# Kernel tuning notes

Measured on AMD Instinct MI355X. Metric: run time of the kernel, lower is better.

The kernel has to match this reference:

```python
import jax, jax.numpy as jnp
import numpy as np

E = 512      # embed_dim
H = 256      # hidden_dim
NH = 4       # num_heads
NC = 5       # num_classes
DH = H // NH # head_dim


def layer_norm(x, g, b, eps=1e-5):
    mu = jnp.mean(x, axis=-1, keepdims=True)
    var = jnp.mean((x - mu) ** 2, axis=-1, keepdims=True)
    return (x - mu) * jax.lax.rsqrt(var + eps) * g + b


def mha_seq1(q_in, kv_in, in_w, in_b, out_w, out_b):
    # q_in, kv_in: [B, H]; in_w: [3H, H]; seq_len == 1 for both query and key/value.
    wq, wk, wv = jnp.split(in_w, 3, axis=0)
    bq, bk, bv = jnp.split(in_b, 3, axis=0)
    B = q_in.shape[0]
    q = (q_in @ wq.T + bq).reshape(B, NH, DH)
    k = (kv_in @ wk.T + bk).reshape(B, NH, DH)
    v = (kv_in @ wv.T + bv).reshape(B, NH, DH)
    scores = jnp.sum(q * k, axis=-1) / jnp.sqrt(jnp.asarray(DH, q.dtype))  # [B, NH]
    w = jax.nn.softmax(scores[..., None], axis=-1)  # [B, NH, 1] (softmax over 1 key == 1)
    attn = (w * v).reshape(B, H)                    # [B, H]
    out = attn @ out_w.T + out_b
    weights = jnp.mean(w, axis=1)[:, None, :]       # [B, 1, 1], averaged over heads
    return out, weights


def setup_inputs() -> dict:
    key = jax.random.key(0)
    ks = jax.random.split(key, 16)
    s = lambda n: 1.0 / np.sqrt(n)
    d = {
        "image_feat": jax.random.normal(ks[0], (65536, E), jnp.float32),
        "text_feat": jax.random.normal(ks[1], (65536, E), jnp.float32),
        "img_proj_w": jax.random.normal(ks[2], (H, E), jnp.float32) * s(E),
        "img_proj_b": jnp.zeros((H,), jnp.float32),
        "txt_proj_w": jax.random.normal(ks[3], (H, E), jnp.float32) * s(E),
        "txt_proj_b": jnp.zeros((H,), jnp.float32),
        "t2i_in_w": jax.random.normal(ks[4], (3 * H, H), jnp.float32) * s(H),
        "t2i_in_b": jnp.zeros((3 * H,), jnp.float32),
        "t2i_out_w": jax.random.normal(ks[5], (H, H), jnp.float32) * s(H),
        "t2i_out_b": jnp.zeros((H,), jnp.float32),
        "i2t_in_w": jax.random.normal(ks[6], (3 * H, H), jnp.float32) * s(H),
        "i2t_in_b": jnp.zeros((3 * H,), jnp.float32),
        "i2t_out_w": jax.random.normal(ks[7], (H, H), jnp.float32) * s(H),
        "i2t_out_b": jnp.zeros((H,), jnp.float32),
        "norm1_g": jnp.ones((H,), jnp.float32),
        "norm1_b": jnp.zeros((H,), jnp.float32),
        "norm2_g": jnp.ones((H,), jnp.float32),
        "norm2_b": jnp.zeros((H,), jnp.float32),
        "cls_ln_g": jnp.ones((2 * H,), jnp.float32),
        "cls_ln_b": jnp.zeros((2 * H,), jnp.float32),
        "cls_w1": jax.random.normal(ks[8], (H, 2 * H), jnp.float32) * s(2 * H),
        "cls_b1": jnp.zeros((H,), jnp.float32),
        "cls_w2": jax.random.normal(ks[9], (NC, H), jnp.float32) * s(H),
        "cls_b2": jnp.zeros((NC,), jnp.float32),
    }
    return d


def reference(image_feat, text_feat, img_proj_w, img_proj_b, txt_proj_w, txt_proj_b,
              t2i_in_w, t2i_in_b, t2i_out_w, t2i_out_b,
              i2t_in_w, i2t_in_b, i2t_out_w, i2t_out_b,
              norm1_g, norm1_b, norm2_g, norm2_b,
              cls_ln_g, cls_ln_b, cls_w1, cls_b1, cls_w2, cls_b2):
    img = image_feat @ img_proj_w.T + img_proj_b   # [B, H]
    txt = text_feat @ txt_proj_w.T + txt_proj_b    # [B, H]
    txt_attn, txt_weights = mha_seq1(txt, img, t2i_in_w, t2i_in_b, t2i_out_w, t2i_out_b)
    txt_attn = layer_norm(txt + txt_attn, norm1_g, norm1_b)
    img_attn, img_weights = mha_seq1(img, txt, i2t_in_w, i2t_in_b, i2t_out_w, i2t_out_b)
    img_attn = layer_norm(img + img_attn, norm2_g, norm2_b)
    fused = jnp.concatenate([txt_attn, img_attn], axis=-1)  # [B, 2H]
    h = layer_norm(fused, cls_ln_g, cls_ln_b)
    h = jax.nn.gelu(h @ cls_w1.T + cls_b1, approximate=False)  # dropout is identity in eval
    out = h @ cls_w2.T + cls_b2                                 # [B, NC]
    return (out, txt_weights, img_weights)
```

## Files before the change

### kernel.cpp

```cpp
#include <hip/hip_runtime.h>
#include <cstdint>
#include <cstddef>


typedef unsigned short u16;
typedef __attribute__((ext_vector_type(8))) short bf16x8;
typedef __attribute__((ext_vector_type(4))) float f32x4;

__device__ __forceinline__ float bf2f(u16 u) {
  union { unsigned int i; float f; } v; v.i = ((unsigned int)u) << 16; return v.f;
}
__device__ __forceinline__ u16 f2bf(float f) {
  union { float f; unsigned int i; } v; v.f = f;
  unsigned int r = v.i + 0x7FFFu + ((v.i >> 16) & 1u);
  return (u16)(r >> 16);
}
__device__ __forceinline__ float ldf(const void* b, long long i, int bf) {
  if (bf) return bf2f(((const u16*)b)[i]);
  return ((const float*)b)[i];
}
__device__ __forceinline__ uint4 load8(const void* base, long long eoff, int bf) {
  if (bf) return *(const uint4*)((const u16*)base + eoff);
  const float* p = (const float*)base + eoff;
  float4 a = *(const float4*)p;
  float4 b = *(const float4*)(p + 4);
  union { u16 h[8]; uint4 u; } t;
  t.h[0] = f2bf(a.x); t.h[1] = f2bf(a.y); t.h[2] = f2bf(a.z); t.h[3] = f2bf(a.w);
  t.h[4] = f2bf(b.x); t.h[5] = f2bf(b.y); t.h[6] = f2bf(b.z); t.h[7] = f2bf(b.w);
  return t.u;
}

__global__ void kd_detect(const void* probe, int* flag) {
  if (threadIdx.x == 0 && blockIdx.x == 0) {
    unsigned int w = *(const unsigned int*)probe;
    *flag = (w == 0x3F803F80u) ? 1 : 0;
  }
}

__global__ void k0_T(const void* t2i_w, const void* i2t_w,
                     const void* img_w, const void* txt_w,
                     const void* img_b, const void* txt_b,
                     const void* t2i_b, const void* i2t_b,
                     float* __restrict__ T, float* __restrict__ cv, const int* dflag)
{
  const int bf = *dflag;
  int t = blockIdx.x * 256 + threadIdx.x;
  int mat = t >> 17;
  int j = (t >> 9) & 255;
  int k = t & 511;
  const void* wv = mat ? i2t_w : t2i_w;
  const void* wp = mat ? txt_w : img_w;
  float s = 0.f;
  #pragma unroll 8
  for (int i = 0; i < 256; ++i)
    s += ldf(wv, 512 * 256 + j * 256 + i, bf) * ldf(wp, i * 512 + k, bf);
  T[(size_t)t] = s;
  if (t < 512) {
    int m2 = t >> 8, j2 = t & 255;
    const void* wv2 = m2 ? i2t_w : t2i_w;
    const void* pb  = m2 ? txt_b : img_b;
    const void* ib  = m2 ? i2t_b : t2i_b;
    float s2 = 0.f;
    for (int i = 0; i < 256; ++i)
      s2 += ldf(wv2, 512 * 256 + j2 * 256 + i, bf) * ldf(pb, i, bf);
    cv[t] = s2 + ldf(ib, 512 + j2, bf);
  }
}

__global__ void k1_P(const void* txt_w, const void* img_w,
                     const void* t2i_ow, const void* i2t_ow,
                     const void* txt_b, const void* img_b,
                     const void* t2i_ob, const void* i2t_ob,
                     const float* __restrict__ T, const float* __restrict__ cv,
                     u16* __restrict__ P, float* __restrict__ c, const int* dflag)
{
  const int bf = *dflag;
  int t = blockIdx.x * 256 + threadIdx.x;
  int n = t >> 10;
  int k = t & 1023;
  u16 val;
  if (n < 256) {
    if (k < 512) {
      val = f2bf(ldf(txt_w, n * 512 + k, bf));
    } else {
      int kk = k - 512;
      float s = 0.f;
      #pragma unroll 8
      for (int j = 0; j < 256; ++j) s += ldf(t2i_ow, n * 256 + j, bf) * T[j * 512 + kk];
      val = f2bf(s);
    }
  } else {
    int n2 = n - 256;
    if (k < 512) {
      float s = 0.f;
      #pragma unroll 8
      for (int j = 0; j < 256; ++j) s += ldf(i2t_ow, n2 * 256 + j, bf) * T[256 * 512 + j * 512 + k];
      val = f2bf(s);
    } else {
      val = f2bf(ldf(img_w, n2 * 512 + (k - 512), bf));
    }
  }
  P[(size_t)n * 1024 + k] = val;
  if (k == 0) {
    float s;
    if (n < 256) {
      s = ldf(txt_b, n, bf) + ldf(t2i_ob, n, bf);
      for (int j = 0; j < 256; ++j) s += ldf(t2i_ow, n * 256 + j, bf) * cv[j];
    } else {
      int n2 = n - 256;
      s = ldf(img_b, n2, bf) + ldf(i2t_ob, n2, bf);
      for (int j = 0; j < 256; ++j) s += ldf(i2t_ow, n2 * 256 + j, bf) * cv[256 + j];
    }
    c[n] = s;
  }
}

__global__ __launch_bounds__(512, 4) void k2f(
    const void* txt, const void* img,
    const u16* __restrict__ P, const float* __restrict__ c,
    const void* g1, const void* b1, const void* g2, const void* b2,
    const void* gc, const void* bc,
    const void* W1, const void* b1c, const void* W2, const void* b2c,
    void* out, const int* dflag)
{
  const int bf = *dflag;
  __shared__ __align__(16) union {
    u16 As[64 * 64];
    u16 F[64 * 512];
  } sm;
  __shared__ float cb[512];
  __shared__ float part[8][64][5];

  const int tid = threadIdx.x;
  const int lane = tid & 63, wid = tid >> 6;
  const int fr = lane & 15, fq = lane >> 4;
  const int bm = blockIdx.x;
  const int wn = wid * 64;

  cb[tid] = c[tid];

  f32x4 acc[4][4];
  const f32x4 zero = {0.f, 0.f, 0.f, 0.f};
  #pragma unroll
  for (int i = 0; i < 4; ++i)
    #pragma unroll
    for (int j = 0; j < 4; ++j) acc[i][j] = zero;

  const int arow = tid >> 3, ac16 = tid & 7;
  for (int k0 = 0; k0 < 1024; k0 += 64) {
    const void* src = (k0 < 512) ? txt : img;
    const int kk = k0 & 511;
    {
      uint4 v = load8(src, (long long)(bm * 64 + arow) * 512 + kk + ac16 * 8, bf);
      ((uint4*)sm.As)[arow * 8 + (ac16 ^ (arow & 7))] = v;
    }
    __syncthreads();
    #pragma unroll
    for (int ks = 0; ks < 64; ks += 32) {
      bf16x8 af[4], bfr[4];
      #pragma unroll
      for (int i = 0; i < 4; ++i) {
        int row = i * 16 + fr;
        af[i] = *(const bf16x8*)((const char*)sm.As + row * 128 +
                                 ((ks * 2 + fq * 16) ^ ((row & 7) << 4)));
      }
      #pragma unroll
      for (int j = 0; j < 4; ++j)
        bfr[j] = *(const bf16x8*)&P[(size_t)(wn + j * 16 + fr) * 1024 + k0 + ks + fq * 8];
      #pragma unroll
      for (int i = 0; i < 4; ++i)
        #pragma unroll
        for (int j = 0; j < 4; ++j)
          acc[i][j] = __builtin_amdgcn_mfma_f32_16x16x32_bf16(af[i], bfr[j], acc[i][j], 0, 0, 0);
    }
    __syncthreads();
  }

  float bj[4];
  #pragma unroll
  for (int j = 0; j < 4; ++j) bj[j] = cb[wn + j * 16 + fr];
  #pragma unroll
  for (int i = 0; i < 4; ++i)
    #pragma unroll
    for (int j = 0; j < 4; ++j)
      #pragma unroll
      for (int r = 0; r < 4; ++r)
        sm.F[(size_t)(i * 16 + fq * 4 + r) * 512 + wn + j * 16 + fr] =
            f2bf(acc[i][j][r] + bj[j]);
  __syncthreads();

  const int c0 = lane * 8;
  const void* gh = (lane >= 32) ? g2 : g1;
  const void* bh = (lane >= 32) ? b2 : b1;
  const int hofs = (lane & 31) * 8;
  float ga8[8], ba8[8], gc8[8], bc8[8];
  #pragma unroll
  for (int i = 0; i < 8; ++i) {
    ga8[i] = ldf(gh, hofs + i, bf);
    ba8[i] = ldf(bh, hofs + i, bf);
    gc8[i] = ldf(gc, c0 + i, bf);
    bc8[i] = ldf(bc, c0 + i, bf);
  }
  for (int rr = 0; rr < 8; ++rr) {
    const int row = wid * 8 + rr;
    uint4 raw = *(const uint4*)&sm.F[(size_t)row * 512 + c0];
    const u16* rp = (const u16*)&raw;
    float x[8];
    #pragma unroll
    for (int i = 0; i < 8; ++i) x[i] = bf2f(rp[i]);
    float s = 0.f, ss = 0.f;
    #pragma unroll
    for (int i = 0; i < 8; ++i) { s += x[i]; ss += x[i] * x[i]; }
    #pragma unroll
    for (int m = 1; m <= 16; m <<= 1) { s += __shfl_xor(s, m, 64); ss += __shfl_xor(ss, m, 64); }
    float mu = s * (1.f / 256.f);
    float var = ss * (1.f / 256.f) - mu * mu;
    float rstd = rsqrtf(var + 1e-5f);
    float y[8]; float s2 = 0.f, ss2 = 0.f;
    #pragma unroll
    for (int i = 0; i < 8; ++i) {
      y[i] = (x[i] - mu) * rstd * ga8[i] + ba8[i];
      s2 += y[i]; ss2 += y[i] * y[i];
    }
    #pragma unroll
    for (int m = 1; m <= 32; m <<= 1) { s2 += __shfl_xor(s2, m, 64); ss2 += __shfl_xor(ss2, m, 64); }
    float mu3 = s2 * (1.f / 512.f);
    float var3 = ss2 * (1.f / 512.f) - mu3 * mu3;
    float r3 = rsqrtf(var3 + 1e-5f);
    union { u16 h[8]; uint4 u; } o;
    #pragma unroll
    for (int i = 0; i < 8; ++i)
      o.h[i] = f2bf((y[i] - mu3) * r3 * gc8[i] + bc8[i]);
    *(uint4*)((char*)sm.F + (size_t)row * 1024 + ((lane * 16) ^ ((row & 7) << 4))) = o.u;
  }
  __syncthreads();

  const int wn2 = wid * 32;
  f32x4 a3[4][2];
  #pragma unroll
  for (int i = 0; i < 4; ++i)
    #pragma unroll
    for (int j = 0; j < 2; ++j) a3[i][j] = zero;
  for (int k0 = 0; k0 < 512; k0 += 32) {
    bf16x8 af[4], bfr[2];
    #pragma unroll
    for (int i = 0; i < 4; ++i) {
      int row = i * 16 + fr;
      af[i] = *(const bf16x8*)((const char*)sm.F + (size_t)row * 1024 +
                               ((k0 * 2 + fq * 16) ^ ((row & 7) << 4)));
    }
    #pragma unroll
    for (int j = 0; j < 2; ++j) {
      uint4 t = load8(W1, (long long)(wn2 + j * 16 + fr) * 512 + k0 + fq * 8, bf);
      bfr[j] = *(const bf16x8*)&t;
    }
    #pragma unroll
    for (int i = 0; i < 4; ++i)
      #pragma unroll
      for (int j = 0; j < 2; ++j)
        a3[i][j] = __builtin_amdgcn_mfma_f32_16x16x32_bf16(af[i], bfr[j], a3[i][j], 0, 0, 0);
  }

  float b1f[2], w2f[5][2];
  #pragma unroll
  for (int j = 0; j < 2; ++j) {
    int n2 = wn2 + j * 16 + fr;
    b1f[j] = ldf(b1c, n2, bf);
    #pragma unroll
    for (int cc = 0; cc < 5; ++cc) w2f[cc][j] = ldf(W2, cc * 256 + n2, bf);
  }
  #pragma unroll
  for (int i = 0; i < 4; ++i) {
    #pragma unroll
    for (int r = 0; r < 4; ++r) {
      float h[2];
      #pragma unroll
      for (int j = 0; j < 2; ++j) {
        float v = a3[i][j][r] + b1f[j];
        h[j] = v * 0.5f * (1.f + erff(v * 0.70710678118654752f));
      }
      #pragma unroll
      for (int cc = 0; cc < 5; ++cc) {
        float pp = h[0] * w2f[cc][0] + h[1] * w2f[cc][1];
        pp += __shfl_xor(pp, 1, 64);
        pp += __shfl_xor(pp, 2, 64);
        pp += __shfl_xor(pp, 4, 64);
        pp += __shfl_xor(pp, 8, 64);
        if (fr == 0) part[wid][i * 16 + fq * 4 + r][cc] = pp;
      }
    }
  }
  __syncthreads();
  if (tid < 320) {
    int r = tid / 5, cc = tid % 5;
    float s = ldf(b2c, cc, bf);
    #pragma unroll
    for (int w = 0; w < 8; ++w) s += part[w][r][cc];
    size_t idx = (size_t)(bm * 64 + r) * 5 + cc;
    if (bf) ((u16*)out)[idx] = f2bf(s);
    else    ((float*)out)[idx] = s;
  }
}

__global__ void k5_w(void* out, const int* dflag) {
  const int bf = *dflag;
  int t = blockIdx.x * 256 + threadIdx.x;
  size_t base = (size_t)5 * 65536;
  if (bf) {
    uint4 v; v.x = v.y = v.z = v.w = 0x3F803F80u;
    *(uint4*)((u16*)out + base + (size_t)t * 8) = v;
  } else {
    float4 one = {1.f, 1.f, 1.f, 1.f};
    float* p = (float*)out + base + (size_t)t * 8;
    *(float4*)p = one;
    *(float4*)(p + 4) = one;
  }
}

extern "C" void kernel_launch(void* const* d_in, const int* in_sizes, int n_in,
                              void* d_out, int out_size, void* d_ws, size_t ws_size,
                              hipStream_t stream)
{
  const void* image_feat = d_in[0];
  const void* text_feat  = d_in[1];
  const void* img_proj_w = d_in[2];
  const void* img_proj_b = d_in[3];
  const void* txt_proj_w = d_in[4];
  const void* txt_proj_b = d_in[5];
  const void* t2i_in_w   = d_in[6];
  const void* t2i_in_b   = d_in[7];
  const void* t2i_out_w  = d_in[8];
  const void* t2i_out_b  = d_in[9];
  const void* i2t_in_w   = d_in[10];
  const void* i2t_in_b   = d_in[11];
  const void* i2t_out_w  = d_in[12];
  const void* i2t_out_b  = d_in[13];
  const void* norm1_g    = d_in[14];
  const void* norm1_b    = d_in[15];
  const void* norm2_g    = d_in[16];
  const void* norm2_b    = d_in[17];
  const void* cls_ln_g   = d_in[18];
  const void* cls_ln_b   = d_in[19];
  const void* cls_w1     = d_in[20];
  const void* cls_b1     = d_in[21];
  const void* cls_w2     = d_in[22];
  const void* cls_b2     = d_in[23];

  char* ws = (char*)d_ws;
  int*   flag = (int*)   (ws + 0);
  u16*   P    = (u16*)   (ws + 1024);
  float* c    = (float*) (ws + 1024 + 1048576);
  float* T    = (float*) (ws + 1051648);
  float* cv   = (float*) (ws + 2100224);

  kd_detect<<<1, 64, 0, stream>>>(norm1_g, flag);
  k0_T<<<1024, 256, 0, stream>>>(t2i_in_w, i2t_in_w, img_proj_w, txt_proj_w,
                                 img_proj_b, txt_proj_b, t2i_in_b, i2t_in_b, T, cv, flag);
  k1_P<<<2048, 256, 0, stream>>>(txt_proj_w, img_proj_w, t2i_out_w, i2t_out_w,
                                 txt_proj_b, img_proj_b, t2i_out_b, i2t_out_b, T, cv, P, c, flag);
  k2f<<<1024, 512, 0, stream>>>(text_feat, image_feat, P, c,
                                norm1_g, norm1_b, norm2_g, norm2_b,
                                cls_ln_g, cls_ln_b,
                                cls_w1, cls_b1, cls_w2, cls_b2, d_out, flag);
  k5_w<<<64, 256, 0, stream>>>(d_out, flag);
}
```

Measured before the change: 612.8 us.

## Tile weight-folding GEMMs and shrink main kernel row tile with register prefetch

The naive per-element weight-precompute kernels are replaced with shared-memory tiled fp32 GEMMs that use far fewer blocks, and bias vectors are computed with parallel reductions. The main fused kernel now handles 32 rows per block instead of 64, doubling the grid. It double-buffers the A tile and prefetches the next A chunk into registers so the per-iteration barrier count drops to one. The LayerNorm and classifier staging buffer gets an XOR swizzle and shares memory with the partial-sum buffer, trading more B-fragment global reloads per row for better occupancy and overlap.

```diff
diff --git a/kernel.cpp b/kernel.cpp
--- a/kernel.cpp
+++ b/kernel.cpp
@@ -29,6 +29,20 @@
   t.h[4] = f2bf(b.x); t.h[5] = f2bf(b.y); t.h[6] = f2bf(b.z); t.h[7] = f2bf(b.w);
   return t.u;
 }
+__device__ __forceinline__ void ld8(const void* base, long long eoff, int bf, float* o) {
+  if (bf) {
+    uint4 v = *(const uint4*)((const u16*)base + eoff);
+    const u16* h = (const u16*)&v;
+    #pragma unroll
+    for (int i = 0; i < 8; ++i) o[i] = bf2f(h[i]);
+  } else {
+    const float* p = (const float*)base + eoff;
+    float4 a = *(const float4*)p;
+    float4 b = *(const float4*)(p + 4);
+    o[0] = a.x; o[1] = a.y; o[2] = a.z; o[3] = a.w;
+    o[4] = b.x; o[5] = b.y; o[6] = b.z; o[7] = b.w;
+  }
+}
 
 __global__ void kd_detect(const void* probe, int* flag) {
   if (threadIdx.x == 0 && blockIdx.x == 0) {
@@ -37,81 +51,157 @@
   }
 }
 
-__global__ void k0_T(const void* t2i_w, const void* i2t_w,
-                     const void* img_w, const void* txt_w,
-                     const void* img_b, const void* txt_b,
-                     const void* t2i_b, const void* i2t_b,
-                     float* __restrict__ T, float* __restrict__ cv, const int* dflag)
+__global__ __launch_bounds__(256) void kp0(
+    const void* t2i_w, const void* i2t_w, const void* img_w, const void* txt_w,
+    const void* img_b, const void* txt_b, const void* t2i_b, const void* i2t_b,
+    float* __restrict__ T, float* __restrict__ cv, const int* dflag)
 {
   const int bf = *dflag;
-  int t = blockIdx.x * 256 + threadIdx.x;
-  int mat = t >> 17;
-  int j = (t >> 9) & 255;
-  int k = t & 511;
+  __shared__ float As_[64][33];
+  __shared__ float Bs_[32][68];
+  __shared__ float red[64][4];
+  const int bid = blockIdx.x;
+  const int mat = bid >> 5, jt = (bid >> 3) & 3, kt = bid & 7;
   const void* wv = mat ? i2t_w : t2i_w;
   const void* wp = mat ? txt_w : img_w;
-  float s = 0.f;
-  #pragma unroll 8
-  for (int i = 0; i < 256; ++i)
-    s += ldf(wv, 512 * 256 + j * 256 + i, bf) * ldf(wp, i * 512 + k, bf);
-  T[(size_t)t] = s;
-  if (t < 512) {
-    int m2 = t >> 8, j2 = t & 255;
-    const void* wv2 = m2 ? i2t_w : t2i_w;
-    const void* pb  = m2 ? txt_b : img_b;
-    const void* ib  = m2 ? i2t_b : t2i_b;
-    float s2 = 0.f;
-    for (int i = 0; i < 256; ++i)
-      s2 += ldf(wv2, 512 * 256 + j2 * 256 + i, bf) * ldf(pb, i, bf);
-    cv[t] = s2 + ldf(ib, 512 + j2, bf);
-  }
-}
-
-__global__ void k1_P(const void* txt_w, const void* img_w,
-                     const void* t2i_ow, const void* i2t_ow,
-                     const void* txt_b, const void* img_b,
-                     const void* t2i_ob, const void* i2t_ob,
-                     const float* __restrict__ T, const float* __restrict__ cv,
-                     u16* __restrict__ P, float* __restrict__ c, const int* dflag)
+  const int tid = threadIdx.x;
+  const int tr = tid >> 4, tc = tid & 15;
+  float acc[4][4];
+  #pragma unroll
+  for (int u = 0; u < 4; ++u)
+    #pragma unroll
+    for (int v = 0; v < 4; ++v) acc[u][v] = 0.f;
+
+  for (int k0 = 0; k0 < 256; k0 += 32) {
+    __syncthreads();
+    #pragma unroll
+    for (int e = 0; e < 8; ++e) {
+      int idx = tid + e * 256;
+      As_[idx >> 5][idx & 31] =
+          ldf(wv, 512 * 256 + (jt * 64 + (idx >> 5)) * 256 + k0 + (idx & 31), bf);
+      Bs_[idx >> 6][idx & 63] =
+          ldf(wp, (long long)(k0 + (idx >> 6)) * 512 + kt * 64 + (idx & 63), bf);
+    }
+    __syncthreads();
+    #pragma unroll
+    for (int kk = 0; kk < 32; ++kk) {
+      float a[4], b[4];
+      #pragma unroll
+      for (int u = 0; u < 4; ++u) a[u] = As_[tr * 4 + u][kk];
+      #pragma unroll
+      for (int v = 0; v < 4; ++v) b[v] = Bs_[kk][tc * 4 + v];
+      #pragma unroll
+      for (int u = 0; u < 4; ++u)
+        #pragma unroll
+        for (int v = 0; v < 4; ++v) acc[u][v] += a[u] * b[v];
+    }
+  }
+  #pragma unroll
+  for (int u = 0; u < 4; ++u)
+    #pragma unroll
+    for (int v = 0; v < 4; ++v)
+      T[(size_t)(mat * 256 + jt * 64 + tr * 4 + u) * 512 + kt * 64 + tc * 4 + v] = acc[u][v];
+
+  if (kt == 0) {
+    const void* pb = mat ? txt_b : img_b;
+    const void* ib = mat ? i2t_b : t2i_b;
+    const int r = tid >> 2, q = tid & 3;
+    float s = 0.f;
+    for (int i = q * 64; i < q * 64 + 64; ++i)
+      s += ldf(wv, 512 * 256 + (jt * 64 + r) * 256 + i, bf) * ldf(pb, i, bf);
+    red[r][q] = s;
+    __syncthreads();
+    if (tid < 64)
+      cv[mat * 256 + jt * 64 + tid] = red[tid][0] + red[tid][1] + red[tid][2] + red[tid][3]
+                                      + ldf(ib, 512 + jt * 64 + tid, bf);
+  }
+}
+
+__global__ __launch_bounds__(256) void kp1(
+    const void* txt_w, const void* img_w,
+    const void* t2i_ow, const void* i2t_ow,
+    const void* txt_b, const void* img_b,
+    const void* t2i_ob, const void* i2t_ob,
+    const float* __restrict__ T, const float* __restrict__ cv,
+    u16* __restrict__ P, float* __restrict__ c, const int* dflag)
 {
   const int bf = *dflag;
-  int t = blockIdx.x * 256 + threadIdx.x;
-  int n = t >> 10;
-  int k = t & 1023;
-  u16 val;
-  if (n < 256) {
-    if (k < 512) {
-      val = f2bf(ldf(txt_w, n * 512 + k, bf));
-    } else {
-      int kk = k - 512;
-      float s = 0.f;
-      #pragma unroll 8
-      for (int j = 0; j < 256; ++j) s += ldf(t2i_ow, n * 256 + j, bf) * T[j * 512 + kk];
-      val = f2bf(s);
+  __shared__ float As_[64][33];
+  __shared__ float Bs_[32][68];
+  __shared__ float red[64][4];
+  const int bid = blockIdx.x, tid = threadIdx.x;
+
+  if (bid < 64) {
+    const int mat = bid >> 5, nt = (bid >> 3) & 3, kt = bid & 7;
+    const void* ow = mat ? i2t_ow : t2i_ow;
+    const float* Tm = T + (size_t)mat * 131072;
+    const int tr = tid >> 4, tc = tid & 15;
+    float acc[4][4];
+    #pragma unroll
+    for (int u = 0; u < 4; ++u)
+      #pragma unroll
+      for (int v = 0; v < 4; ++v) acc[u][v] = 0.f;
+    for (int j0 = 0; j0 < 256; j0 += 32) {
+      __syncthreads();
+      #pragma unroll
+      for (int e = 0; e < 8; ++e) {
+        int idx = tid + e * 256;
+        As_[idx >> 5][idx & 31] =
+            ldf(ow, (nt * 64 + (idx >> 5)) * 256 + j0 + (idx & 31), bf);
+        Bs_[idx >> 6][idx & 63] = Tm[(size_t)(j0 + (idx >> 6)) * 512 + kt * 64 + (idx & 63)];
+      }
+      __syncthreads();
+      #pragma unroll
+      for (int kk = 0; kk < 32; ++kk) {
+        float a[4], b[4];
+        #pragma unroll
+        for (int u = 0; u < 4; ++u) a[u] = As_[tr * 4 + u][kk];
+        #pragma unroll
+        for (int v = 0; v < 4; ++v) b[v] = Bs_[kk][tc * 4 + v];
+        #pragma unroll
+        for (int u = 0; u < 4; ++u)
+          #pragma unroll
+          for (int v = 0; v < 4; ++v) acc[u][v] += a[u] * b[v];
+      }
+    }
+    #pragma unroll
+    for (int u = 0; u < 4; ++u)
+      #pragma unroll
+      for (int v = 0; v < 4; ++v) {
+        int n = nt * 64 + tr * 4 + u, k = kt * 64 + tc * 4 + v;
+        if (mat == 0) P[(size_t)n * 1024 + 512 + k] = f2bf(acc[u][v]);
+        else          P[(size_t)(256 + n) * 1024 + k] = f2bf(acc[u][v]);
+      }
+  } else if (bid < 80) {
+    const int cb_ = bid - 64, mat = cb_ >> 3, rt = cb_ & 7;
+    #pragma unroll 4
+    for (int e = 0; e < 64; ++e) {
+      int idx = tid + e * 256;
+      int r = idx >> 9, cc2 = idx & 511;
+      if (mat == 0)
+        P[(size_t)(rt * 32 + r) * 1024 + cc2] =
+            f2bf(ldf(txt_w, (long long)(rt * 32 + r) * 512 + cc2, bf));
+      else
+        P[(size_t)(256 + rt * 32 + r) * 1024 + 512 + cc2] =
+            f2bf(ldf(img_w, (long long)(rt * 32 + r) * 512 + cc2, bf));
     }
   } else {
-    int n2 = n - 256;
-    if (k < 512) {
-      float s = 0.f;
-      #pragma unroll 8
-      for (int j = 0; j < 256; ++j) s += ldf(i2t_ow, n2 * 256 + j, bf) * T[256 * 512 + j * 512 + k];
-      val = f2bf(s);
-    } else {
-      val = f2bf(ldf(img_w, n2 * 512 + (k - 512), bf));
-    }
-  }
-  P[(size_t)n * 1024 + k] = val;
-  if (k == 0) {
-    float s;
-    if (n < 256) {
-      s = ldf(txt_b, n, bf) + ldf(t2i_ob, n, bf);
-      for (int j = 0; j < 256; ++j) s += ldf(t2i_ow, n * 256 + j, bf) * cv[j];
-    } else {
-      int n2 = n - 256;
-      s = ldf(img_b, n2, bf) + ldf(i2t_ob, n2, bf);
-      for (int j = 0; j < 256; ++j) s += ldf(i2t_ow, n2 * 256 + j, bf) * cv[256 + j];
-    }
-    c[n] = s;
+    const int cb2 = bid - 80;
+    const int n0 = cb2 * 64;
+    const int half = n0 >> 8;
+    const void* ow  = half ? i2t_ow : t2i_ow;
+    const void* pb2 = half ? img_b  : txt_b;
+    const void* ob  = half ? i2t_ob : t2i_ob;
+    const int nh = n0 & 255;
+    const int r = tid >> 2, q = tid & 3;
+    float s = 0.f;
+    for (int j = q * 64; j < q * 64 + 64; ++j)
+      s += ldf(ow, (nh + r) * 256 + j, bf) * cv[half * 256 + j];
+    red[r][q] = s;
+    __syncthreads();
+    if (tid < 64)
+      c[n0 + tid] = red[tid][0] + red[tid][1] + red[tid][2] + red[tid][3]
+                    + ldf(pb2, nh + tid, bf) + ldf(ob, nh + tid, bf);
   }
 }
 
@@ -125,11 +215,11 @@
 {
   const int bf = *dflag;
   __shared__ __align__(16) union {
-    u16 As[64 * 64];
-    u16 F[64 * 512];
+    u16 As[2 * 32 * 64];
+    u16 F[32 * 512];
+    float part[8][32][5];
   } sm;
   __shared__ float cb[512];
-  __shared__ float part[8][64][5];
 
   const int tid = threadIdx.x;
   const int lane = tid & 63, wid = tid >> 6;
@@ -139,71 +229,81 @@
 
   cb[tid] = c[tid];
 
-  f32x4 acc[4][4];
+  f32x4 acc[2][4];
   const f32x4 zero = {0.f, 0.f, 0.f, 0.f};
   #pragma unroll
-  for (int i = 0; i < 4; ++i)
+  for (int i = 0; i < 2; ++i)
     #pragma unroll
     for (int j = 0; j < 4; ++j) acc[i][j] = zero;
 
   const int arow = tid >> 3, ac16 = tid & 7;
+  const long long zrow = (long long)(bm * 32 + arow) * 512 + ac16 * 8;
+  uint4 zv;
+  if (tid < 256) zv = load8(txt, zrow, bf);
+  int buf = 0;
   for (int k0 = 0; k0 < 1024; k0 += 64) {
-    const void* src = (k0 < 512) ? txt : img;
-    const int kk = k0 & 511;
-    {
-      uint4 v = load8(src, (long long)(bm * 64 + arow) * 512 + kk + ac16 * 8, bf);
-      ((uint4*)sm.As)[arow * 8 + (ac16 ^ (arow & 7))] = v;
+    if (tid < 256)
+      ((uint4*)sm.As)[buf * 256 + arow * 8 + (ac16 ^ (arow & 7))] = zv;
+    bf16x8 b0[4], b1f_[4];
+    #pragma unroll
+    for (int j = 0; j < 4; ++j) {
+      const u16* pp = &P[(size_t)(wn + j * 16 + fr) * 1024 + k0 + fq * 8];
+      b0[j]   = *(const bf16x8*)pp;
+      b1f_[j] = *(const bf16x8*)(pp + 32);
     }
     __syncthreads();
-    #pragma unroll
-    for (int ks = 0; ks < 64; ks += 32) {
-      bf16x8 af[4], bfr[4];
-      #pragma unroll
-      for (int i = 0; i < 4; ++i) {
-        int row = i * 16 + fr;
-        af[i] = *(const bf16x8*)((const char*)sm.As + row * 128 +
-                                 ((ks * 2 + fq * 16) ^ ((row & 7) << 4)));
-      }
+    if (tid < 256 && k0 + 64 < 1024) {
+      const void* nsrc = (k0 + 64 < 512) ? txt : img;
+      zv = load8(nsrc, zrow + ((k0 + 64) & 511), bf);
+    }
+    bf16x8 a0[2], a1[2];
+    #pragma unroll
+    for (int i = 0; i < 2; ++i) {
+      int row = i * 16 + fr;
+      const char* base = (const char*)sm.As + buf * 4096 + row * 128;
+      a0[i] = *(const bf16x8*)(base + ((fq * 16) ^ ((row & 7) << 4)));
+      a1[i] = *(const bf16x8*)(base + ((64 + fq * 16) ^ ((row & 7) << 4)));
+    }
+    #pragma unroll
+    for (int i = 0; i < 2; ++i)
       #pragma unroll
       for (int j = 0; j < 4; ++j)
-        bfr[j] = *(const bf16x8*)&P[(size_t)(wn + j * 16 + fr) * 1024 + k0 + ks + fq * 8];
-      #pragma unroll
-      for (int i = 0; i < 4; ++i)
-        #pragma unroll
-        for (int j = 0; j < 4; ++j)
-          acc[i][j] = __builtin_amdgcn_mfma_f32_16x16x32_bf16(af[i], bfr[j], acc[i][j], 0, 0, 0);
-    }
-    __syncthreads();
-  }
+        acc[i][j] = __builtin_amdgcn_mfma_f32_16x16x32_bf16(a0[i], b0[j], acc[i][j], 0, 0, 0);
+    #pragma unroll
+    for (int i = 0; i < 2; ++i)
+      #pragma unroll
+      for (int j = 0; j < 4; ++j)
+        acc[i][j] = __builtin_amdgcn_mfma_f32_16x16x32_bf16(a1[i], b1f_[j], acc[i][j], 0, 0, 0);
+    buf ^= 1;
+  }
+  __syncthreads();
 
   float bj[4];
   #pragma unroll
   for (int j = 0; j < 4; ++j) bj[j] = cb[wn + j * 16 + fr];
   #pragma unroll
-  for (int i = 0; i < 4; ++i)
+  for (int i = 0; i < 2; ++i)
     #pragma unroll
     for (int j = 0; j < 4; ++j)
       #pragma unroll
-      for (int r = 0; r < 4; ++r)
-        sm.F[(size_t)(i * 16 + fq * 4 + r) * 512 + wn + j * 16 + fr] =
-            f2bf(acc[i][j][r] + bj[j]);
+      for (int r = 0; r < 4; ++r) {
+        int row = i * 16 + fq * 4 + r;
+        int col = wn + j * 16 + fr;
+        int g = (col >> 3) ^ (row & 7);
+        sm.F[row * 512 + g * 8 + (col & 7)] = f2bf(acc[i][j][r] + bj[j]);
+      }
   __syncthreads();
 
   const int c0 = lane * 8;
-  const void* gh = (lane >= 32) ? g2 : g1;
-  const void* bh = (lane >= 32) ? b2 : b1;
-  const int hofs = (lane & 31) * 8;
   float ga8[8], ba8[8], gc8[8], bc8[8];
-  #pragma unroll
-  for (int i = 0; i < 8; ++i) {
-    ga8[i] = ldf(gh, hofs + i, bf);
-    ba8[i] = ldf(bh, hofs + i, bf);
-    gc8[i] = ldf(gc, c0 + i, bf);
-    bc8[i] = ldf(bc, c0 + i, bf);
-  }
-  for (int rr = 0; rr < 8; ++rr) {
-    const int row = wid * 8 + rr;
-    uint4 raw = *(const uint4*)&sm.F[(size_t)row * 512 + c0];
+  ld8((lane >= 32) ? g2 : g1, (lane & 31) * 8, bf, ga8);
+  ld8((lane >= 32) ? b2 : b1, (lane & 31) * 8, bf, ba8);
+  ld8(gc, c0, bf, gc8);
+  ld8(bc, c0, bf, bc8);
+  #pragma unroll 2
+  for (int rr = 0; rr < 4; ++rr) {
+    const int row = wid * 4 + rr;
+    uint4 raw = ((const uint4*)sm.F)[row * 64 + (lane ^ (row & 7))];
     const u16* rp = (const u16*)&raw;
     float x[8];
     #pragma unroll
@@ -231,35 +331,37 @@
     #pragma unroll
     for (int i = 0; i < 8; ++i)
       o.h[i] = f2bf((y[i] - mu3) * r3 * gc8[i] + bc8[i]);
-    *(uint4*)((char*)sm.F + (size_t)row * 1024 + ((lane * 16) ^ ((row & 7) << 4))) = o.u;
+    ((uint4*)sm.F)[row * 64 + (lane ^ (row & 7))] = o.u;
   }
   __syncthreads();
 
   const int wn2 = wid * 32;
-  f32x4 a3[4][2];
-  #pragma unroll
-  for (int i = 0; i < 4; ++i)
+  f32x4 a3[2][2];
+  #pragma unroll
+  for (int i = 0; i < 2; ++i)
     #pragma unroll
     for (int j = 0; j < 2; ++j) a3[i][j] = zero;
+  #pragma unroll 2
   for (int k0 = 0; k0 < 512; k0 += 32) {
-    bf16x8 af[4], bfr[2];
-    #pragma unroll
-    for (int i = 0; i < 4; ++i) {
-      int row = i * 16 + fr;
-      af[i] = *(const bf16x8*)((const char*)sm.F + (size_t)row * 1024 +
-                               ((k0 * 2 + fq * 16) ^ ((row & 7) << 4)));
-    }
+    bf16x8 bw[2], af[2];
     #pragma unroll
     for (int j = 0; j < 2; ++j) {
       uint4 t = load8(W1, (long long)(wn2 + j * 16 + fr) * 512 + k0 + fq * 8, bf);
-      bfr[j] = *(const bf16x8*)&t;
-    }
-    #pragma unroll
-    for (int i = 0; i < 4; ++i)
+      bw[j] = *(const bf16x8*)&t;
+    }
+    #pragma unroll
+    for (int i = 0; i < 2; ++i) {
+      int row = i * 16 + fr;
+      int g = ((k0 >> 3) + fq) ^ (row & 7);
+      af[i] = *(const bf16x8*)&sm.F[row * 512 + g * 8];
+    }
+    #pragma unroll
+    for (int i = 0; i < 2; ++i)
       #pragma unroll
       for (int j = 0; j < 2; ++j)
-        a3[i][j] = __builtin_amdgcn_mfma_f32_16x16x32_bf16(af[i], bfr[j], a3[i][j], 0, 0, 0);
-  }
+        a3[i][j] = __builtin_amdgcn_mfma_f32_16x16x32_bf16(af[i], bw[j], a3[i][j], 0, 0, 0);
+  }
+  __syncthreads();
 
   float b1f[2], w2f[5][2];
   #pragma unroll
@@ -270,7 +372,7 @@
     for (int cc = 0; cc < 5; ++cc) w2f[cc][j] = ldf(W2, cc * 256 + n2, bf);
   }
   #pragma unroll
-  for (int i = 0; i < 4; ++i) {
+  for (int i = 0; i < 2; ++i) {
     #pragma unroll
     for (int r = 0; r < 4; ++r) {
       float h[2];
@@ -286,17 +388,17 @@
         pp += __shfl_xor(pp, 2, 64);
         pp += __shfl_xor(pp, 4, 64);
         pp += __shfl_xor(pp, 8, 64);
-        if (fr == 0) part[wid][i * 16 + fq * 4 + r][cc] = pp;
+        if (fr == 0) sm.part[wid][i * 16 + fq * 4 + r][cc] = pp;
       }
     }
   }
   __syncthreads();
-  if (tid < 320) {
+  if (tid < 160) {
     int r = tid / 5, cc = tid % 5;
     float s = ldf(b2c, cc, bf);
     #pragma unroll
-    for (int w = 0; w < 8; ++w) s += part[w][r][cc];
-    size_t idx = (size_t)(bm * 64 + r) * 5 + cc;
+    for (int w = 0; w < 8; ++w) s += sm.part[w][r][cc];
+    size_t idx = (size_t)(bm * 32 + r) * 5 + cc;
     if (bf) ((u16*)out)[idx] = f2bf(s);
     else    ((float*)out)[idx] = s;
   }
@@ -354,11 +456,12 @@
   float* cv   = (float*) (ws + 2100224);
 
   kd_detect<<<1, 64, 0, stream>>>(norm1_g, flag);
-  k0_T<<<1024, 256, 0, stream>>>(t2i_in_w, i2t_in_w, img_proj_w, txt_proj_w,
-                                 img_proj_b, txt_proj_b, t2i_in_b, i2t_in_b, T, cv, flag);
-  k1_P<<<2048, 256, 0, stream>>>(txt_proj_w, img_proj_w, t2i_out_w, i2t_out_w,
-                                 txt_proj_b, img_proj_b, t2i_out_b, i2t_out_b, T, cv, P, c, flag);
-  k2f<<<1024, 512, 0, stream>>>(text_feat, image_feat, P, c,
+  kp0<<<64, 256, 0, stream>>>(t2i_in_w, i2t_in_w, img_proj_w, txt_proj_w,
+                              img_proj_b, txt_proj_b, t2i_in_b, i2t_in_b, T, cv, flag);
+  kp1<<<88, 256, 0, stream>>>(txt_proj_w, img_proj_w, t2i_out_w, i2t_out_w,
+                              txt_proj_b, img_proj_b, t2i_out_b, i2t_out_b,
+                              T, cv, P, c, flag);
+  k2f<<<2048, 512, 0, stream>>>(text_feat, image_feat, P, c,
                                 norm1_g, norm1_b, norm2_g, norm2_b,
                                 cls_ln_g, cls_ln_b,
                                 cls_w1, cls_b1, cls_w2, cls_b2, d_out, flag);
```

New measurement: 709.2 us. 15.7% more time.
